# Performance work log

Hardware: AMD Instinct MI355X
Metric: run time of the kernel (lower is better)

Reference implementation:

```python
import jax, jax.numpy as jnp
import numpy as np

NUM_HEADS = 32
NUM_KV_HEADS = 8
HEAD_DIM = 128


def rotate_half(x):
    half = x.shape[-1] // 2
    return jnp.concatenate([-x[..., half:], x[..., :half]], axis=-1)


def setup_inputs() -> dict:
    key = jax.random.key(0)
    ks = jax.random.split(key, 7)
    B, S, H = 2, 2048, 4096
    hidden_states = jax.random.normal(ks[0], (B, S, H), dtype=jnp.float32)
    # rope tables built from real frequencies for realism
    inv_freq = 1.0 / (10000.0 ** (jnp.arange(0, HEAD_DIM, 2, dtype=jnp.float32) / HEAD_DIM))
    pos = jnp.arange(S, dtype=jnp.float32)
    freqs = pos[:, None] * inv_freq[None, :]            # [S, HEAD_DIM//2]
    emb = jnp.concatenate([freqs, freqs], axis=-1)      # [S, HEAD_DIM]
    cos = jnp.broadcast_to(jnp.cos(emb)[None], (B, S, HEAD_DIM)).astype(jnp.float32)
    sin = jnp.broadcast_to(jnp.sin(emb)[None], (B, S, HEAD_DIM)).astype(jnp.float32)
    scale = 0.02
    wq = jax.random.normal(ks[1], (NUM_HEADS * HEAD_DIM, H), dtype=jnp.float32) * scale
    wk = jax.random.normal(ks[2], (NUM_KV_HEADS * HEAD_DIM, H), dtype=jnp.float32) * scale
    wv = jax.random.normal(ks[3], (NUM_KV_HEADS * HEAD_DIM, H), dtype=jnp.float32) * scale
    wo = jax.random.normal(ks[4], (H, NUM_HEADS * HEAD_DIM), dtype=jnp.float32) * scale
    return {"hidden_states": hidden_states, "cos": cos, "sin": sin,
            "wq": wq, "wk": wk, "wv": wv, "wo": wo}


def reference(hidden_states, cos, sin, wq, wk, wv, wo):
    B, S, H = hidden_states.shape
    groups = NUM_HEADS // NUM_KV_HEADS
    scaling = HEAD_DIM ** -0.5

    # QKV projections (nn.Linear, no bias -> x @ W^T)
    q = (hidden_states @ wq.T).reshape(B, S, NUM_HEADS, HEAD_DIM).transpose(0, 2, 1, 3)     # [B,Hq,S,D]
    k = (hidden_states @ wk.T).reshape(B, S, NUM_KV_HEADS, HEAD_DIM).transpose(0, 2, 1, 3)  # [B,Hk,S,D]
    v = (hidden_states @ wv.T).reshape(B, S, NUM_KV_HEADS, HEAD_DIM).transpose(0, 2, 1, 3)  # [B,Hk,S,D]

    # RoPE (HF apply_rotary_pos_emb: cos/sin unsqueezed over head axis)
    c = cos[:, None, :, :]  # [B,1,S,D]
    s = sin[:, None, :, :]
    q = q * c + rotate_half(q) * s
    k = k * c + rotate_half(k) * s

    # GQA: broadcast each KV head to its group of query heads
    k = jnp.repeat(k, groups, axis=1)  # [B,Hq,S,D]
    v = jnp.repeat(v, groups, axis=1)

    # causal SDPA
    scores = jnp.einsum('bhqd,bhkd->bhqk', q, k) * scaling
    causal = jnp.tril(jnp.ones((S, S), dtype=bool))
    neg = jnp.finfo(scores.dtype).min
    scores = jnp.where(causal[None, None], scores, neg)
    probs = jax.nn.softmax(scores, axis=-1)
    attn = jnp.einsum('bhqk,bhkd->bhqd', probs, v)      # [B,Hq,S,D]

    # merge heads + output projection
    attn = attn.transpose(0, 2, 1, 3).reshape(B, S, NUM_HEADS * HEAD_DIM)
    return attn @ wo.T
```

## Files before the change

### kernel.cpp

```cpp
#include <hip/hip_runtime.h>
#include <stdint.h>

typedef __bf16 bf16_t;
typedef __bf16 bf16x8 __attribute__((ext_vector_type(8)));
typedef __bf16 bf16x4 __attribute__((ext_vector_type(4)));
typedef float f32x4 __attribute__((ext_vector_type(4)));

#define S_LEN 2048
#define NH 32
#define NKV 8
#define HD 128
#define B_SZ 2
#define HID 4096
#define QKV_N 6144
#define INFF __builtin_inff()

__device__ __forceinline__ void gload_lds16(const void* g, void* l) {
    __builtin_amdgcn_global_load_lds(
        (const __attribute__((address_space(1))) void*)(uintptr_t)g,
        (__attribute__((address_space(3))) void*)(uint32_t)(uintptr_t)l,
        16, 0, 0);
}

__global__ __launch_bounds__(256) void f2b_kernel(const float4* __restrict__ in,
                                                  bf16x4* __restrict__ out, int n4) {
    int i = blockIdx.x * blockDim.x + threadIdx.x;
    if (i >= n4) return;
    float4 v = in[i];
    bf16x4 o = {(bf16_t)v.x, (bf16_t)v.y, (bf16_t)v.z, (bf16_t)v.w};
    out[i] = o;
}

#define SLOT_E 16384

#define GTILE(T, STAGE, VMW) do {                                                         \
    const int _sb = ((T) & 3) * SLOT_E;                                                   \
    bf16x8 af[8], bfr[2];                                                                 \
    _Pragma("unroll") for (int i = 0; i < 8; ++i)                                         \
        af[i] = *(const bf16x8*)&lds[_sb + offA[i]];                                      \
    bfr[0] = *(const bf16x8*)&lds[_sb + 8192 + offB[0]];                                  \
    bfr[1] = *(const bf16x8*)&lds[_sb + 8192 + offB[1]];                                  \
    if (STAGE) {                                                                          \
        const int _ss = (((T) + 3) & 3) * SLOT_E;                                         \
        gload_lds16(sA0, &lds[_ss + ldsO0]); gload_lds16(sA1, &lds[_ss + ldsO1]);         \
        sA0 += 32; sA1 += 32;                                                             \
    }                                                                                     \
    __builtin_amdgcn_s_barrier();                                                         \
    asm volatile("s_waitcnt lgkmcnt(0)" ::: "memory");                                    \
    __builtin_amdgcn_sched_barrier(0);                                                    \
    __builtin_amdgcn_s_setprio(1);                                                        \
    _Pragma("unroll") for (int i = 0; i < 8; ++i) {                                       \
        acc[i][0] = __builtin_amdgcn_mfma_f32_16x16x32_bf16(af[i], bfr[0], acc[i][0], 0, 0, 0); \
        acc[i][1] = __builtin_amdgcn_mfma_f32_16x16x32_bf16(af[i], bfr[1], acc[i][1], 0, 0, 0); \
    }                                                                                     \
    __builtin_amdgcn_s_setprio(0);                                                        \
    __builtin_amdgcn_s_barrier();                                                         \
    bf16x8 bfs[2];                                                                        \
    bfs[0] = *(const bf16x8*)&lds[_sb + 8192 + offB[2]];                                  \
    bfs[1] = *(const bf16x8*)&lds[_sb + 8192 + offB[3]];                                  \
    if (STAGE) {                                                                          \
        const int _ss = (((T) + 3) & 3) * SLOT_E;                                         \
        gload_lds16(sB0, &lds[_ss + 8192 + ldsO0]); gload_lds16(sB1, &lds[_ss + 8192 + ldsO1]); \
        sB0 += 32; sB1 += 32;                                                             \
    }                                                                                     \
    __builtin_amdgcn_s_barrier();                                                         \
    asm volatile("s_waitcnt lgkmcnt(0)" ::: "memory");                                    \
    __builtin_amdgcn_sched_barrier(0);                                                    \
    __builtin_amdgcn_s_setprio(1);                                                        \
    _Pragma("unroll") for (int i = 0; i < 8; ++i) {                                       \
        acc[i][2] = __builtin_amdgcn_mfma_f32_16x16x32_bf16(af[i], bfs[0], acc[i][2], 0, 0, 0); \
        acc[i][3] = __builtin_amdgcn_mfma_f32_16x16x32_bf16(af[i], bfs[1], acc[i][3], 0, 0, 0); \
    }                                                                                     \
    __builtin_amdgcn_s_setprio(0);                                                        \
    if ((VMW) == 8)      asm volatile("s_waitcnt vmcnt(8)" ::: "memory");                 \
    else if ((VMW) == 4) asm volatile("s_waitcnt vmcnt(4)" ::: "memory");                 \
    else if ((VMW) == 0) asm volatile("s_waitcnt vmcnt(0)" ::: "memory");                 \
    __builtin_amdgcn_s_barrier();                                                         \
} while (0)

template<bool F32OUT>
__global__ __launch_bounds__(512, 2) void gemm256(const bf16_t* __restrict__ A,
                                                  const bf16_t* __restrict__ W,
                                                  void* __restrict__ C0,
                                                  void* __restrict__ C1,
                                                  int ld0, int ld1,
                                                  int Nloc, int ldAW, int Kloc) {
    __shared__ __align__(16) bf16_t lds[4 * SLOT_E];
    const int tid = threadIdx.x;
    const int lane = tid & 63;
    const int w = tid >> 6;
    const int wm = w >> 2, wn = w & 3;
    const int l15 = lane & 15, lg = lane >> 4;

    const int z = blockIdx.y;
    void* Cv = z ? C1 : C0;
    const int ldC = z ? ld1 : ld0;
    const int kOff = z * Kloc;

    const int nbx = Nloc >> 8;
    const int cpx = gridDim.x >> 3;
    const int bid = blockIdx.x;
    const int bid2 = (bid & 7) * cpx + (bid >> 3);
    const int m0 = (bid2 / nbx) * 256;
    const int n0 = (bid2 % nbx) * 256;

    const int c0 = tid, c1 = 512 + tid;
    const int rA0 = c0 >> 2, ch0 = (c0 & 3) ^ ((rA0 >> 1) & 3);
    const int rA1 = c1 >> 2, ch1 = (c1 & 3) ^ ((rA1 >> 1) & 3);
    const bf16_t* sA0 = A + (size_t)(m0 + rA0) * ldAW + kOff + ch0 * 8;
    const bf16_t* sA1 = A + (size_t)(m0 + rA1) * ldAW + kOff + ch1 * 8;
    const bf16_t* sB0 = W + (size_t)(n0 + rA0) * ldAW + kOff + ch0 * 8;
    const bf16_t* sB1 = W + (size_t)(n0 + rA1) * ldAW + kOff + ch1 * 8;
    const int ldsO0 = c0 * 8, ldsO1 = c1 * 8;

    int offA[8], offB[4];
    #pragma unroll
    for (int i = 0; i < 8; ++i) {
        int row = wm * 128 + i * 16 + l15;
        offA[i] = row * 32 + ((lg ^ ((row >> 1) & 3)) * 8);
    }
    #pragma unroll
    for (int j = 0; j < 4; ++j) {
        int row = wn * 64 + j * 16 + l15;
        offB[j] = row * 32 + ((lg ^ ((row >> 1) & 3)) * 8);
    }

    #pragma unroll
    for (int tt = 0; tt < 3; ++tt) {
        const int ss = tt * SLOT_E;
        gload_lds16(sA0, &lds[ss + ldsO0]); gload_lds16(sA1, &lds[ss + ldsO1]);
        gload_lds16(sB0, &lds[ss + 8192 + ldsO0]); gload_lds16(sB1, &lds[ss + 8192 + ldsO1]);
        sA0 += 32; sA1 += 32; sB0 += 32; sB1 += 32;
    }
    asm volatile("s_waitcnt vmcnt(8)" ::: "memory");
    __builtin_amdgcn_s_barrier();

    f32x4 acc[8][4] = {};
    const int NT = Kloc >> 5;
    int t = 0;
    for (; t < NT - 3; ++t) GTILE(t, true, 8);
    GTILE(NT - 3, false, 4);
    GTILE(NT - 2, false, 0);
    GTILE(NT - 1, false, -1);

    #pragma unroll
    for (int i = 0; i < 8; ++i)
        #pragma unroll
        for (int jn = 0; jn < 4; ++jn)
            #pragma unroll
            for (int r = 0; r < 4; ++r) {
                int m = m0 + wm * 128 + i * 16 + lg * 4 + r;
                int n = n0 + wn * 64 + jn * 16 + l15;
                float v = acc[i][jn][r];
                if (F32OUT) ((float*)Cv)[(size_t)m * ldC + n] = v;
                else        ((bf16_t*)Cv)[(size_t)m * ldC + n] = (bf16_t)v;
            }
}

__global__ __launch_bounds__(256) void rope_fuse(bf16_t* __restrict__ QKV,
                                                 const bf16_t* __restrict__ P1,
                                                 const float* __restrict__ cosb,
                                                 const float* __restrict__ sinb) {
    int tid = blockIdx.x * blockDim.x + threadIdx.x;
    int d = tid & 63;
    int hg = (tid >> 6) % 48;
    int bs = tid / (64 * 48);
    bf16_t* rowp;
    float x1, x2;
    if (hg < 32) {
        rowp = QKV + (size_t)bs * QKV_N + hg * HD;
        x1 = (float)rowp[d];
        x2 = (float)rowp[d + 64];
    } else if (hg < 40) {
        int col = HID + (hg - 32) * HD;
        rowp = QKV + (size_t)bs * QKV_N + col;
        const bf16_t* pp = P1 + (size_t)bs * 2048 + (col - HID);
        x1 = (float)rowp[d] + (float)pp[d];
        x2 = (float)rowp[d + 64] + (float)pp[d + 64];
    } else {
        int col = HID + NKV * HD + (hg - 40) * HD;
        rowp = QKV + (size_t)bs * QKV_N + col;
        const bf16_t* pp = P1 + (size_t)bs * 2048 + (col - HID);
        rowp[d]      = (bf16_t)((float)rowp[d]      + (float)pp[d]);
        rowp[d + 64] = (bf16_t)((float)rowp[d + 64] + (float)pp[d + 64]);
        return;
    }
    float c1 = cosb[(size_t)bs * HD + d];
    float s1 = sinb[(size_t)bs * HD + d];
    float c2 = cosb[(size_t)bs * HD + d + 64];
    float s2 = sinb[(size_t)bs * HD + d + 64];
    rowp[d]      = (bf16_t)(x1 * c1 - x2 * s1);
    rowp[d + 64] = (bf16_t)(x2 * c2 + x1 * s2);
}

#define PITCH_P 72

__global__ __launch_bounds__(256, 2) void attn_fwd(const bf16_t* __restrict__ QKV,
                                                   bf16_t* __restrict__ O) {
    __shared__ __align__(16) bf16_t Kl[2][64 * 128];
    __shared__ __align__(16) bf16_t Vt[2][128 * 64];
    __shared__ __align__(16) bf16_t Pl[4][16 * PITCH_P];
    const int tid = threadIdx.x;
    const int lane = tid & 63;
    const int w = tid >> 6;
    const int l15 = lane & 15, lg = lane >> 4;
    const int pr = blockIdx.x, h = blockIdx.y, b = blockIdx.z;
    const int kvh = h >> 2;
    const float scale = 0.08838834764831845f;

    int krow[4], kch[4];
    for (int jj = 0; jj < 4; ++jj) { int q = jj * 256 + tid; krow[jj] = q >> 4; kch[jj] = q & 15; }
    const int d0 = (tid >> 4) * 8;
    const int k0v = (tid & 15) * 4;
    const int vci = k0v >> 3;
    const int vsub = k0v & 7;

    const bf16_t* Kb0 = QKV + (size_t)(b * S_LEN) * QKV_N + HID + kvh * HD;
    const bf16_t* Vb0 = QKV + (size_t)(b * S_LEN) * QKV_N + HID + NKV * HD + kvh * HD;
    bf16_t* Plw = Pl[w];

    for (int t = 0; t < 2; ++t) {
        const int qt = (t == 0) ? pr : (31 - pr);
        const int q0 = qt * 64;
        const int qrow = q0 + w * 16 + l15;

        bf16x8 qf[4];
        {
            const bf16_t* qp = QKV + (size_t)(b * S_LEN + qrow) * QKV_N + h * HD;
            for (int c = 0; c < 4; ++c) qf[c] = *(const bf16x8*)&qp[c * 32 + lg * 8];
        }

        f32x4 acc_o[8] = {};
        float mrow = -INFF, lrow = 0.f;
        const int nsteps = qt + 1;

        bf16x8 kst[4], vst[4];
        for (int jj = 0; jj < 4; ++jj)
            kst[jj] = *(const bf16x8*)&Kb0[(size_t)krow[jj] * QKV_N + kch[jj] * 8];
        for (int j2 = 0; j2 < 4; ++j2)
            vst[j2] = *(const bf16x8*)&Vb0[(size_t)(k0v + j2) * QKV_N + d0];

        __syncthreads();

        for (int st = 0; st < nsteps; ++st) {
            const int k0 = st * 64;
            const int p = st & 1;
            for (int jj = 0; jj < 4; ++jj)
                *(bf16x8*)&Kl[p][krow[jj] * 128 + ((kch[jj] ^ (krow[jj] & 7)) * 8)] = kst[jj];
            #pragma unroll
            for (int j = 0; j < 8; ++j) {
                bf16x4 cvec = { vst[0][j], vst[1][j], vst[2][j], vst[3][j] };
                *(bf16x4*)&Vt[p][(d0 + j) * 64 + ((vci ^ j) << 3) + vsub] = cvec;
            }
            __syncthreads();
            if (st + 1 < nsteps) {
                const bf16_t* Kb = Kb0 + (size_t)(k0 + 64) * QKV_N;
                const bf16_t* Vb = Vb0 + (size_t)(k0 + 64) * QKV_N;
                for (int jj = 0; jj < 4; ++jj)
                    kst[jj] = *(const bf16x8*)&Kb[(size_t)krow[jj] * QKV_N + kch[jj] * 8];
                for (int j2 = 0; j2 < 4; ++j2)
                    vst[j2] = *(const bf16x8*)&Vb[(size_t)(k0v + j2) * QKV_N + d0];
            }
            f32x4 s[4];
            #pragma unroll
            for (int nt = 0; nt < 4; ++nt) {
                s[nt] = (f32x4){0.f, 0.f, 0.f, 0.f};
                const int row = nt * 16 + l15;
                const int rb = row * 128, key = row & 7;
                #pragma unroll
                for (int c = 0; c < 4; ++c) {
                    bf16x8 kf = *(const bf16x8*)&Kl[p][rb + (((c * 4 + lg) ^ key) * 8)];
                    s[nt] = __builtin_amdgcn_mfma_f32_16x16x32_bf16(kf, qf[c], s[nt], 0, 0, 0);
                }
            }
            float ev[4][4];
            float mx = -INFF;
            #pragma unroll
            for (int nt = 0; nt < 4; ++nt)
                #pragma unroll
                for (int r = 0; r < 4; ++r) {
                    int k = k0 + nt * 16 + lg * 4 + r;
                    float v = (k <= qrow) ? s[nt][r] * scale : -INFF;
                    ev[nt][r] = v;
                    mx = fmaxf(mx, v);
                }
            mx = fmaxf(mx, __shfl_xor(mx, 16));
            mx = fmaxf(mx, __shfl_xor(mx, 32));
            const bool nodefer = !__all(mx <= mrow + 8.f);
            float mn, sc;
            if (nodefer) { mn = fmaxf(mrow, mx); sc = __expf(mrow - mn); }
            else         { mn = mrow;            sc = 1.f; }
            float rs = 0.f;
            #pragma unroll
            for (int nt = 0; nt < 4; ++nt)
                #pragma unroll
                for (int r = 0; r < 4; ++r) {
                    float e = __expf(ev[nt][r] - mn);
                    ev[nt][r] = e; rs += e;
                }
            rs += __shfl_xor(rs, 16);
            rs += __shfl_xor(rs, 32);
            mrow = mn;
            lrow = lrow * sc + rs;
            #pragma unroll
            for (int nt = 0; nt < 4; ++nt) {
                bf16x4 pk = {(bf16_t)ev[nt][0], (bf16_t)ev[nt][1], (bf16_t)ev[nt][2], (bf16_t)ev[nt][3]};
                *(bf16x4*)&Plw[l15 * PITCH_P + nt * 16 + lg * 4] = pk;
            }
            if (nodefer) {
                float scb[4];
                #pragma unroll
                for (int r = 0; r < 4; ++r) scb[r] = __shfl(sc, lg * 4 + r);
                #pragma unroll
                for (int nt2 = 0; nt2 < 8; ++nt2)
                    #pragma unroll
                    for (int r = 0; r < 4; ++r) acc_o[nt2][r] *= scb[r];
            }
            #pragma unroll
            for (int kc = 0; kc < 2; ++kc) {
                bf16x8 pf = *(const bf16x8*)&Plw[l15 * PITCH_P + kc * 32 + lg * 8];
                #pragma unroll
                for (int nt2 = 0; nt2 < 8; ++nt2) {
                    const int drow = nt2 * 16 + l15;
                    bf16x8 vf = *(const bf16x8*)&Vt[p][drow * 64 + (((kc * 4 + lg) ^ (drow & 7)) << 3)];
                    acc_o[nt2] = __builtin_amdgcn_mfma_f32_16x16x32_bf16(pf, vf, acc_o[nt2], 0, 0, 0);
                }
            }
        }
        float lb[4];
        #pragma unroll
        for (int r = 0; r < 4; ++r) lb[r] = __shfl(lrow, lg * 4 + r);
        #pragma unroll
        for (int nt2 = 0; nt2 < 8; ++nt2)
            #pragma unroll
            for (int r = 0; r < 4; ++r) {
                int q = q0 + w * 16 + lg * 4 + r;
                int d = nt2 * 16 + l15;
                O[((size_t)(b * S_LEN + q)) * (NH * HD) + h * HD + d] = (bf16_t)(acc_o[nt2][r] / lb[r]);
            }
    }
}

extern "C" void kernel_launch(void* const* d_in, const int* in_sizes, int n_in,
                              void* d_out, int out_size, void* d_ws, size_t ws_size,
                              hipStream_t stream) {
    const float* hs   = (const float*)d_in[0];
    const float* cosb = (const float*)d_in[1];
    const float* sinb = (const float*)d_in[2];
    const float* wq   = (const float*)d_in[3];
    const float* wk   = (const float*)d_in[4];
    const float* wv   = (const float*)d_in[5];
    const float* wo   = (const float*)d_in[6];
    float* out = (float*)d_out;

    const size_t NHS = (size_t)B_SZ * S_LEN * HID;
    const size_t NQKVW = (size_t)QKV_N * HID;
    size_t need = (NHS * 3 + NQKVW * 2) * sizeof(bf16_t);
    if (ws_size < need) return;

    bf16_t* p = (bf16_t*)d_ws;
    bf16_t* hsb  = p; p += NHS;
    bf16_t* wqkv = p; p += NQKVW;
    bf16_t* wob  = p; p += NHS;
    bf16_t* QKVb = p; p += NQKVW;
    bf16_t* Ab   = p; p += NHS;
    bf16_t* P1   = Ab;

    auto cvt = [&](const float* src, bf16_t* dst, size_t n) {
        int n4 = (int)(n / 4);
        f2b_kernel<<<(n4 + 255) / 256, 256, 0, stream>>>((const float4*)src, (bf16x4*)dst, n4);
    };
    cvt(hs, hsb, NHS);
    cvt(wq, wqkv, NHS);
    cvt(wk, wqkv + (size_t)HID * HID, (size_t)NKV * HD * HID);
    cvt(wv, wqkv + (size_t)(HID + NKV * HD) * HID, (size_t)NKV * HD * HID);
    cvt(wo, wob, NHS);

    gemm256<false><<<dim3(256, 1), 512, 0, stream>>>(hsb, wqkv, QKVb, QKVb,
                                                     QKV_N, QKV_N, 4096, HID, HID);
    gemm256<false><<<dim3(128, 2), 512, 0, stream>>>(hsb, wqkv + (size_t)HID * HID,
                                                     QKVb + HID, P1,
                                                     QKV_N, 2048, 2048, HID, 2048);

    int rf_threads = B_SZ * S_LEN * 48 * 64;
    rope_fuse<<<rf_threads / 256, 256, 0, stream>>>(QKVb, P1, cosb, sinb);

    attn_fwd<<<dim3(16, NH, B_SZ), 256, 0, stream>>>(QKVb, Ab);

    gemm256<true><<<dim3(256, 1), 512, 0, stream>>>(Ab, wob, out, out,
                                                    HID, HID, HID, HID, HID);
}
```

Measured before the change: 563.7 us.

## Use 128-row query tiles with 8 waves and fold softmax scale into Q

```diff
diff --git a/kernel.cpp b/kernel.cpp
--- a/kernel.cpp
+++ b/kernel.cpp
@@ -4,6 +4,7 @@
 typedef __bf16 bf16_t;
 typedef __bf16 bf16x8 __attribute__((ext_vector_type(8)));
 typedef __bf16 bf16x4 __attribute__((ext_vector_type(4)));
+typedef __bf16 bf16x2 __attribute__((ext_vector_type(2)));
 typedef float f32x4 __attribute__((ext_vector_type(4)));
 
 #define S_LEN 2048
@@ -14,6 +15,7 @@
 #define HID 4096
 #define QKV_N 6144
 #define INFF __builtin_inff()
+#define QSCALE (0.08838834764831845f * 1.4426950408889634f)
 
 __device__ __forceinline__ void gload_lds16(const void* g, void* l) {
     __builtin_amdgcn_global_load_lds(
@@ -166,11 +168,12 @@
     int hg = (tid >> 6) % 48;
     int bs = tid / (64 * 48);
     bf16_t* rowp;
-    float x1, x2;
+    float x1, x2, posc = 1.f;
     if (hg < 32) {
         rowp = QKV + (size_t)bs * QKV_N + hg * HD;
         x1 = (float)rowp[d];
         x2 = (float)rowp[d + 64];
+        posc = QSCALE;
     } else if (hg < 40) {
         int col = HID + (hg - 32) * HD;
         rowp = QKV + (size_t)bs * QKV_N + col;
@@ -189,77 +192,80 @@
     float s1 = sinb[(size_t)bs * HD + d];
     float c2 = cosb[(size_t)bs * HD + d + 64];
     float s2 = sinb[(size_t)bs * HD + d + 64];
-    rowp[d]      = (bf16_t)(x1 * c1 - x2 * s1);
-    rowp[d + 64] = (bf16_t)(x2 * c2 + x1 * s2);
-}
-
-#define PITCH_P 72
-
-__global__ __launch_bounds__(256, 2) void attn_fwd(const bf16_t* __restrict__ QKV,
+    rowp[d]      = (bf16_t)((x1 * c1 - x2 * s1) * posc);
+    rowp[d + 64] = (bf16_t)((x2 * c2 + x1 * s2) * posc);
+}
+
+__device__ __forceinline__ int vkeyf(int d) { return (d & 7) ^ (((d >> 3) & 3) << 1); }
+
+__global__ __launch_bounds__(512, 4) void attn_fwd(const bf16_t* __restrict__ QKV,
                                                    bf16_t* __restrict__ O) {
     __shared__ __align__(16) bf16_t Kl[2][64 * 128];
     __shared__ __align__(16) bf16_t Vt[2][128 * 64];
-    __shared__ __align__(16) bf16_t Pl[4][16 * PITCH_P];
+    __shared__ __align__(16) bf16_t Pl[8][16 * 64];
     const int tid = threadIdx.x;
     const int lane = tid & 63;
     const int w = tid >> 6;
     const int l15 = lane & 15, lg = lane >> 4;
     const int pr = blockIdx.x, h = blockIdx.y, b = blockIdx.z;
     const int kvh = h >> 2;
-    const float scale = 0.08838834764831845f;
-
-    int krow[4], kch[4];
-    for (int jj = 0; jj < 4; ++jj) { int q = jj * 256 + tid; krow[jj] = q >> 4; kch[jj] = q & 15; }
-    const int d0 = (tid >> 4) * 8;
-    const int k0v = (tid & 15) * 4;
-    const int vci = k0v >> 3;
-    const int vsub = k0v & 7;
+
+    int krow[2], kch[2];
+    for (int jj = 0; jj < 2; ++jj) { int q = jj * 512 + tid; krow[jj] = q >> 4; kch[jj] = q & 15; }
+    const int k0v = (tid & 31) * 2;
+    const int d0 = (tid >> 5) * 8;
+    const int pkey = l15 & 7;
 
     const bf16_t* Kb0 = QKV + (size_t)(b * S_LEN) * QKV_N + HID + kvh * HD;
     const bf16_t* Vb0 = QKV + (size_t)(b * S_LEN) * QKV_N + HID + NKV * HD + kvh * HD;
     bf16_t* Plw = Pl[w];
 
     for (int t = 0; t < 2; ++t) {
-        const int qt = (t == 0) ? pr : (31 - pr);
-        const int q0 = qt * 64;
+        const int qt = (t == 0) ? pr : (15 - pr);
+        const int q0 = qt * 128;
         const int qrow = q0 + w * 16 + l15;
 
         bf16x8 qf[4];
         {
             const bf16_t* qp = QKV + (size_t)(b * S_LEN + qrow) * QKV_N + h * HD;
+            #pragma unroll
             for (int c = 0; c < 4; ++c) qf[c] = *(const bf16x8*)&qp[c * 32 + lg * 8];
         }
 
         f32x4 acc_o[8] = {};
         float mrow = -INFF, lrow = 0.f;
-        const int nsteps = qt + 1;
-
-        bf16x8 kst[4], vst[4];
-        for (int jj = 0; jj < 4; ++jj)
+        const int nsteps = 2 * qt + 2;
+
+        bf16x8 kst[2], vst[2];
+        #pragma unroll
+        for (int jj = 0; jj < 2; ++jj)
             kst[jj] = *(const bf16x8*)&Kb0[(size_t)krow[jj] * QKV_N + kch[jj] * 8];
-        for (int j2 = 0; j2 < 4; ++j2)
-            vst[j2] = *(const bf16x8*)&Vb0[(size_t)(k0v + j2) * QKV_N + d0];
+        vst[0] = *(const bf16x8*)&Vb0[(size_t)(k0v + 0) * QKV_N + d0];
+        vst[1] = *(const bf16x8*)&Vb0[(size_t)(k0v + 1) * QKV_N + d0];
 
         __syncthreads();
 
         for (int st = 0; st < nsteps; ++st) {
             const int k0 = st * 64;
             const int p = st & 1;
-            for (int jj = 0; jj < 4; ++jj)
+            #pragma unroll
+            for (int jj = 0; jj < 2; ++jj)
                 *(bf16x8*)&Kl[p][krow[jj] * 128 + ((kch[jj] ^ (krow[jj] & 7)) * 8)] = kst[jj];
             #pragma unroll
             for (int j = 0; j < 8; ++j) {
-                bf16x4 cvec = { vst[0][j], vst[1][j], vst[2][j], vst[3][j] };
-                *(bf16x4*)&Vt[p][(d0 + j) * 64 + ((vci ^ j) << 3) + vsub] = cvec;
+                bf16x2 pr2 = { vst[0][j], vst[1][j] };
+                const int d = d0 + j;
+                *(bf16x2*)&Vt[p][d * 64 + (((k0v >> 3) ^ vkeyf(d)) * 8) + (k0v & 7)] = pr2;
             }
             __syncthreads();
             if (st + 1 < nsteps) {
                 const bf16_t* Kb = Kb0 + (size_t)(k0 + 64) * QKV_N;
                 const bf16_t* Vb = Vb0 + (size_t)(k0 + 64) * QKV_N;
-                for (int jj = 0; jj < 4; ++jj)
+                #pragma unroll
+                for (int jj = 0; jj < 2; ++jj)
                     kst[jj] = *(const bf16x8*)&Kb[(size_t)krow[jj] * QKV_N + kch[jj] * 8];
-                for (int j2 = 0; j2 < 4; ++j2)
-                    vst[j2] = *(const bf16x8*)&Vb[(size_t)(k0v + j2) * QKV_N + d0];
+                vst[0] = *(const bf16x8*)&Vb[(size_t)(k0v + 0) * QKV_N + d0];
+                vst[1] = *(const bf16x8*)&Vb[(size_t)(k0v + 1) * QKV_N + d0];
             }
             f32x4 s[4];
             #pragma unroll
@@ -273,39 +279,44 @@
                     s[nt] = __builtin_amdgcn_mfma_f32_16x16x32_bf16(kf, qf[c], s[nt], 0, 0, 0);
                 }
             }
-            float ev[4][4];
-            float mx = -INFF;
-            #pragma unroll
-            for (int nt = 0; nt < 4; ++nt)
-                #pragma unroll
-                for (int r = 0; r < 4; ++r) {
-                    int k = k0 + nt * 16 + lg * 4 + r;
-                    float v = (k <= qrow) ? s[nt][r] * scale : -INFF;
-                    ev[nt][r] = v;
-                    mx = fmaxf(mx, v);
-                }
+            if (k0 + 63 > q0 + w * 16) {
+                #pragma unroll
+                for (int nt = 0; nt < 4; ++nt)
+                    #pragma unroll
+                    for (int r = 0; r < 4; ++r) {
+                        int k = k0 + nt * 16 + lg * 4 + r;
+                        if (k > qrow) s[nt][r] = -INFF;
+                    }
+            }
+            float m0a = fmaxf(fmaxf(s[0][0], s[0][1]), fmaxf(s[0][2], s[0][3]));
+            float m1a = fmaxf(fmaxf(s[1][0], s[1][1]), fmaxf(s[1][2], s[1][3]));
+            float m2a = fmaxf(fmaxf(s[2][0], s[2][1]), fmaxf(s[2][2], s[2][3]));
+            float m3a = fmaxf(fmaxf(s[3][0], s[3][1]), fmaxf(s[3][2], s[3][3]));
+            float mx = fmaxf(fmaxf(m0a, m1a), fmaxf(m2a, m3a));
             mx = fmaxf(mx, __shfl_xor(mx, 16));
             mx = fmaxf(mx, __shfl_xor(mx, 32));
-            const bool nodefer = !__all(mx <= mrow + 8.f);
-            float mn, sc;
-            if (nodefer) { mn = fmaxf(mrow, mx); sc = __expf(mrow - mn); }
-            else         { mn = mrow;            sc = 1.f; }
-            float rs = 0.f;
-            #pragma unroll
-            for (int nt = 0; nt < 4; ++nt)
-                #pragma unroll
-                for (int r = 0; r < 4; ++r) {
-                    float e = __expf(ev[nt][r] - mn);
-                    ev[nt][r] = e; rs += e;
-                }
+            const bool nodefer = !__all(mx <= mrow + 11.5f);
+            const float mn = nodefer ? fmaxf(mrow, mx) : mrow;
+            float sc = 1.f;
+            if (nodefer) sc = exp2f(mrow - mn);
+            float rs0 = 0.f, rs1 = 0.f, rs2 = 0.f, rs3 = 0.f;
+            #pragma unroll
+            for (int nt = 0; nt < 4; ++nt) {
+                float e0 = exp2f(s[nt][0] - mn), e1 = exp2f(s[nt][1] - mn);
+                float e2 = exp2f(s[nt][2] - mn), e3 = exp2f(s[nt][3] - mn);
+                s[nt][0] = e0; s[nt][1] = e1; s[nt][2] = e2; s[nt][3] = e3;
+                rs0 += e0; rs1 += e1; rs2 += e2; rs3 += e3;
+            }
+            float rs = (rs0 + rs1) + (rs2 + rs3);
             rs += __shfl_xor(rs, 16);
             rs += __shfl_xor(rs, 32);
-            mrow = mn;
-            lrow = lrow * sc + rs;
+            if (nodefer) { lrow = lrow * sc + rs; mrow = mn; }
+            else         { lrow += rs; }
             #pragma unroll
             for (int nt = 0; nt < 4; ++nt) {
-                bf16x4 pk = {(bf16_t)ev[nt][0], (bf16_t)ev[nt][1], (bf16_t)ev[nt][2], (bf16_t)ev[nt][3]};
-                *(bf16x4*)&Plw[l15 * PITCH_P + nt * 16 + lg * 4] = pk;
+                bf16x4 pk = {(bf16_t)s[nt][0], (bf16_t)s[nt][1], (bf16_t)s[nt][2], (bf16_t)s[nt][3]};
+                const int cw = nt * 2 + (lg >> 1);
+                *(bf16x4*)&Plw[l15 * 64 + ((cw ^ pkey) * 8) + (lg & 1) * 4] = pk;
             }
             if (nodefer) {
                 float scb[4];
@@ -318,11 +329,11 @@
             }
             #pragma unroll
             for (int kc = 0; kc < 2; ++kc) {
-                bf16x8 pf = *(const bf16x8*)&Plw[l15 * PITCH_P + kc * 32 + lg * 8];
+                bf16x8 pf = *(const bf16x8*)&Plw[l15 * 64 + (((kc * 4 + lg) ^ pkey) * 8)];
                 #pragma unroll
                 for (int nt2 = 0; nt2 < 8; ++nt2) {
                     const int drow = nt2 * 16 + l15;
-                    bf16x8 vf = *(const bf16x8*)&Vt[p][drow * 64 + (((kc * 4 + lg) ^ (drow & 7)) << 3)];
+                    bf16x8 vf = *(const bf16x8*)&Vt[p][drow * 64 + (((kc * 4 + lg) ^ vkeyf(drow)) * 8)];
                     acc_o[nt2] = __builtin_amdgcn_mfma_f32_16x16x32_bf16(pf, vf, acc_o[nt2], 0, 0, 0);
                 }
             }
@@ -385,7 +396,7 @@
     int rf_threads = B_SZ * S_LEN * 48 * 64;
     rope_fuse<<<rf_threads / 256, 256, 0, stream>>>(QKVb, P1, cosb, sinb);
 
-    attn_fwd<<<dim3(16, NH, B_SZ), 256, 0, stream>>>(QKVb, Ab);
+    attn_fwd<<<dim3(8, NH, B_SZ), 512, 0, stream>>>(QKVb, Ab);
 
     gemm256<true><<<dim3(256, 1), 512, 0, stream>>>(Ab, wob, out, out,
                                                     HID, HID, HID, HID, HID);
```

Result: slower. 701.2 us (+24.4%).
